# Performance work log

Measured on AMD Instinct MI355X. Metric: run time of the kernel, lower is better.

The kernel has to match this reference:

```python
import jax, jax.numpy as jnp
import numpy as np

N = 50000
E = 800000
NUM_GRAPHS = 128
X_IN, HID, EDGE_DIM = 64, 64, 16


def setup_inputs() -> dict:
    key = jax.random.key(0)
    ks = jax.random.split(key, 9)
    s = 0.05
    inp = {
        'x': jax.random.normal(ks[0], (N, X_IN), jnp.float32),
        'edge_index': jax.random.randint(ks[1], (2, E), 0, N, dtype=jnp.int32),
        'edge_attr': jax.random.normal(ks[2], (E, EDGE_DIM), jnp.float32),
        'batch': jnp.sort(jax.random.randint(ks[3], (N,), 0, NUM_GRAPHS, dtype=jnp.int32)),
        'w_fc1': jax.random.normal(ks[4], (EDGE_DIM, 1), jnp.float32) * s,
        'b_fc1': jnp.zeros((1,), jnp.float32),
    }
    dims = [(X_IN, HID), (HID, HID * 2), (HID * 2, HID)]
    for i, (din, dout) in enumerate(dims):
        k1, k2, k3 = jax.random.split(ks[5 + i], 3)
        inp[f'w1_{i}'] = jax.random.normal(k1, (din, dout), jnp.float32) * s
        inp[f'b1_{i}'] = jnp.zeros((dout,), jnp.float32)
        inp[f'w2_{i}'] = jax.random.normal(k2, (din, dout), jnp.float32) * s
        inp[f'w3_{i}'] = jax.random.normal(k3, (din, dout), jnp.float32) * s
        inp[f'b3_{i}'] = jnp.zeros((dout,), jnp.float32)
    return inp


def leconv(x, src, dst, ew, w1, b1, w2, w3, b3):
    # PyG LEConv: out_i = lin3(x_i) + sum_{j->i} e_ji * (lin1(x_j) - lin2(x_i))
    a = x @ w1 + b1          # lin1 (bias=True)   [N, out]
    b = x @ w2               # lin2 (bias=False)  [N, out]
    msg = ew[:, None] * (a[src] - b[dst])          # [E, out]
    agg = jax.ops.segment_sum(msg, dst, num_segments=N)
    return agg + x @ w3 + b3  # lin3 (bias=True)


def reference(x, edge_index, edge_attr, batch,
              w_fc1, b_fc1,
              w1_0, b1_0, w2_0, w3_0, b3_0,
              w1_1, b1_1, w2_1, w3_1, b3_1,
              w1_2, b1_2, w2_2, w3_2, b3_2):
    src, dst = edge_index[0], edge_index[1]
    ew = (edge_attr @ w_fc1 + b_fc1)[:, 0]         # fc1(edge_attr).squeeze(-1) -> [E]
    h = jax.nn.elu(leconv(x, src, dst, ew, w1_0, b1_0, w2_0, w3_0, b3_0))
    h = jax.nn.elu(leconv(h, src, dst, ew, w1_1, b1_1, w2_1, w3_1, b3_1))
    h = jax.nn.elu(leconv(h, src, dst, ew, w1_2, b1_2, w2_2, w3_2, b3_2))
    # global max pool over nodes of each graph -> [NUM_GRAPHS, HID]
    return jax.ops.segment_max(h, batch, num_segments=NUM_GRAPHS)
```

## Files before the change

### kernel.cpp

```cpp
#include <hip/hip_runtime.h>
#include <math.h>

#define N_NODES 50000
#define N_EDGES 800000
#define NUM_GRAPHS_ 128
#define SCAN_NB 98

typedef unsigned short u16;
typedef unsigned int u32;
typedef __attribute__((ext_vector_type(8))) short bf16x8;
typedef __attribute__((ext_vector_type(4))) float f32x4;

__device__ __forceinline__ float elu_f(float v) {
    return v > 0.f ? v : (__expf(v) - 1.f);
}
__device__ __forceinline__ u16 f2bf(float f) {
    u32 u = __float_as_uint(f);
    u += 0x7FFFu + ((u >> 16) & 1u);
    return (u16)(u >> 16);
}
__device__ __forceinline__ float bf2f(u16 h) {
    return __uint_as_float(((u32)h) << 16);
}
__device__ __forceinline__ void bfpair(u32 v, float& lo, float& hi) {
    lo = __uint_as_float(v << 16);
    hi = __uint_as_float(v & 0xFFFF0000u);
}
__device__ __forceinline__ u32 packbf(float lo, float hi) {
    return (u32)f2bf(lo) | ((u32)f2bf(hi) << 16);
}

__global__ void conv_x_kernel(const float* __restrict__ x, u16* __restrict__ xb) {
    int g = blockIdx.x * blockDim.x + threadIdx.x;
    float4 v = ((const float4*)x)[g];
    uint2 o;
    o.x = packbf(v.x, v.y);
    o.y = packbf(v.z, v.w);
    ((uint2*)xb)[g] = o;
}

__global__ void ew_deg_kernel(const float* __restrict__ edge_attr,
                              const float* __restrict__ w_fc1,
                              const float* __restrict__ b_fc1,
                              const int* __restrict__ edge_index,
                              float* __restrict__ ew,
                              int* __restrict__ deg) {
    int e = blockIdx.x * blockDim.x + threadIdx.x;
    if (e >= N_EDGES) return;
    const float4* ea = (const float4*)(edge_attr + (size_t)e * 16);
    const float4* wf = (const float4*)w_fc1;
    float acc = b_fc1[0];
#pragma unroll
    for (int i = 0; i < 4; i++) {
        float4 a = ea[i], w = wf[i];
        acc += a.x * w.x + a.y * w.y + a.z * w.z + a.w * w.w;
    }
    ew[e] = acc;
    atomicAdd(&deg[edge_index[N_EDGES + e]], 1);
}

__global__ void pack_w_kernel(const float* __restrict__ w3_0, const float* __restrict__ w1_0, const float* __restrict__ w2_0,
                              const float* __restrict__ w3_1, const float* __restrict__ w1_1, const float* __restrict__ w2_1,
                              const float* __restrict__ w3_2, const float* __restrict__ w1_2, const float* __restrict__ w2_2,
                              u16* __restrict__ bp0, u16* __restrict__ bp1, u16* __restrict__ bp2) {
    int t = blockIdx.x * blockDim.x + threadIdx.x;
    if (t >= 7680) return;
    int DIN, DOUT, lid;
    const float *w3, *w1, *w2;
    u16* bp;
    if (t < 1536)      { DIN = 64;  DOUT = 64;  lid = t;        w3 = w3_0; w1 = w1_0; w2 = w2_0; bp = bp0; }
    else if (t < 4608) { DIN = 64;  DOUT = 128; lid = t - 1536; w3 = w3_1; w1 = w1_1; w2 = w2_1; bp = bp1; }
    else               { DIN = 128; DOUT = 64;  lid = t - 4608; w3 = w3_2; w1 = w1_2; w2 = w2_2; bp = bp2; }
    const int NT = DOUT / 16;
    const int lane = lid & 63;
    const int fragid = lid >> 6;
    const int chunk = fragid / NT;
    const int ntile = fragid % NT;
    const int n = ntile * 16 + (lane & 15);
    const int kbase = chunk * 32 + (lane >> 4) * 8;
    u16 buf[8];
#pragma unroll
    for (int j = 0; j < 8; j++) {
        int k = kbase + j;
        int region = k / DIN;
        int kk = k - region * DIN;
        float v = (region == 0) ? w3[kk * DOUT + n]
                : (region == 1) ? w1[kk * DOUT + n]
                                : -w2[kk * DOUT + n];
        buf[j] = f2bf(v);
    }
    *(bf16x8*)(bp + ((size_t)lid << 3)) = *(bf16x8*)buf;
}

__global__ __launch_bounds__(256) void scan1_kernel(const int* __restrict__ deg,
                                                    int* __restrict__ rowptr,
                                                    int* __restrict__ blk_sums) {
    __shared__ int sh[256];
    const int t = threadIdx.x;
    const int base = blockIdx.x * 512;
    const int i0 = base + 2 * t, i1 = i0 + 1;
    const int d0 = (i0 < N_NODES) ? deg[i0] : 0;
    const int d1 = (i1 < N_NODES) ? deg[i1] : 0;
    const int pair = d0 + d1;
    int v = pair;
    sh[t] = v;
    __syncthreads();
#pragma unroll
    for (int off = 1; off < 256; off <<= 1) {
        int add = (t >= off) ? sh[t - off] : 0;
        __syncthreads();
        v += add;
        sh[t] = v;
        __syncthreads();
    }
    const int excl = v - pair;
    if (i0 < N_NODES) rowptr[i0] = excl;
    if (i1 < N_NODES) rowptr[i1] = excl + d0;
    if (t == 255) blk_sums[blockIdx.x] = v;
}

__global__ __launch_bounds__(128) void scan2_kernel(const int* __restrict__ blk_sums,
                                                    int* __restrict__ blk_offs,
                                                    int* __restrict__ rowptr) {
    __shared__ int sh[128];
    const int t = threadIdx.x;
    const int orig = (t < SCAN_NB) ? blk_sums[t] : 0;
    int v = orig;
    sh[t] = v;
    __syncthreads();
#pragma unroll
    for (int off = 1; off < 128; off <<= 1) {
        int add = (t >= off) ? sh[t - off] : 0;
        __syncthreads();
        v += add;
        sh[t] = v;
        __syncthreads();
    }
    if (t < SCAN_NB) blk_offs[t] = v - orig;
    if (t == 127) rowptr[N_NODES] = v;
}

__global__ void scan3_kernel(int* __restrict__ rowptr,
                             const int* __restrict__ blk_offs,
                             int* __restrict__ cursor) {
    int i = blockIdx.x * blockDim.x + threadIdx.x;
    if (i >= N_NODES) return;
    int r = rowptr[i] + blk_offs[i >> 9];
    rowptr[i] = r;
    cursor[i] = r;
}

__global__ void place_kernel(const int* __restrict__ edge_index,
                             const float* __restrict__ ew,
                             int* __restrict__ cursor,
                             int2* __restrict__ csr) {
    int e = blockIdx.x * blockDim.x + threadIdx.x;
    if (e >= N_EDGES) return;
    int dst = edge_index[N_EDGES + e];
    int pos = atomicAdd(&cursor[dst], 1);
    int2 ent;
    ent.x = edge_index[e];
    ent.y = __float_as_int(ew[e]);
    csr[pos] = ent;
}

template <int DIN, bool WRITE_C>
__global__ __launch_bounds__(256) void gather_kernel(
    const u16* __restrict__ xb, const int* __restrict__ rowptr,
    const int2* __restrict__ csr, u16* __restrict__ sb,
    u16* __restrict__ chb, float* __restrict__ c) {
    constexpr int CG = DIN / 4;
    constexpr int EG = 64 / CG;
    const int gid = blockIdx.x * 256 + threadIdx.x;
    const int node = gid >> 6;
    if (node >= N_NODES) return;
    const int lane = threadIdx.x & 63;
    const int cg = lane & (CG - 1);
    const int eg = lane / CG;
    const int beg = rowptr[node];
    const int end = rowptr[node + 1];
    const uint2* x2 = (const uint2*)xb;

    float a0 = 0.f, a1 = 0.f, a2 = 0.f, a3 = 0.f;
    float b0 = 0.f, b1 = 0.f, b2 = 0.f, b3 = 0.f;
    float wsum = 0.f;

    int p = beg + eg;
    for (; p + EG < end; p += 2 * EG) {
        int2 e0 = csr[p];
        int2 e1 = csr[p + EG];
        float w0 = __int_as_float(e0.y);
        float w1 = __int_as_float(e1.y);
        uint2 v0 = x2[(size_t)e0.x * CG + cg];
        uint2 v1 = x2[(size_t)e1.x * CG + cg];
        float f0, f1, f2, f3, g0, g1, g2, g3;
        bfpair(v0.x, f0, f1); bfpair(v0.y, f2, f3);
        bfpair(v1.x, g0, g1); bfpair(v1.y, g2, g3);
        a0 += w0 * f0; a1 += w0 * f1; a2 += w0 * f2; a3 += w0 * f3;
        b0 += w1 * g0; b1 += w1 * g1; b2 += w1 * g2; b3 += w1 * g3;
        wsum += w0 + w1;
    }
    if (p < end) {
        int2 e0 = csr[p];
        float w0 = __int_as_float(e0.y);
        uint2 v0 = x2[(size_t)e0.x * CG + cg];
        float f0, f1, f2, f3;
        bfpair(v0.x, f0, f1); bfpair(v0.y, f2, f3);
        a0 += w0 * f0; a1 += w0 * f1; a2 += w0 * f2; a3 += w0 * f3;
        wsum += w0;
    }
    a0 += b0; a1 += b1; a2 += b2; a3 += b3;

#pragma unroll
    for (int off = 32; off >= CG; off >>= 1) {
        a0 += __shfl_xor(a0, off);
        a1 += __shfl_xor(a1, off);
        a2 += __shfl_xor(a2, off);
        a3 += __shfl_xor(a3, off);
        wsum += __shfl_xor(wsum, off);
    }

    if (lane < CG) {
        uint2 so;
        so.x = packbf(a0, a1);
        so.y = packbf(a2, a3);
        ((uint2*)sb)[(size_t)node * CG + cg] = so;
        const float cn = WRITE_C ? wsum : c[node];
        uint2 hv = x2[(size_t)node * CG + cg];
        float h0, h1, h2, h3;
        bfpair(hv.x, h0, h1); bfpair(hv.y, h2, h3);
        uint2 co;
        co.x = packbf(cn * h0, cn * h1);
        co.y = packbf(cn * h2, cn * h3);
        ((uint2*)chb)[(size_t)node * CG + cg] = co;
    }
    if (WRITE_C && lane == 0) c[node] = wsum;
}

template <int DIN, int DOUT>
__global__ __launch_bounds__(256) void gemm_mfma(
    const u16* __restrict__ hb, const u16* __restrict__ sb,
    const u16* __restrict__ chb, const u16* __restrict__ Bp,
    const float* __restrict__ cvec, const float* __restrict__ bias1,
    const float* __restrict__ bias3, u16* __restrict__ outp) {
    constexpr int CH = DIN / 32;
    constexpr int CHUNKS = 3 * CH;
    constexpr int NT = DOUT / 16;
    const int tid = threadIdx.x;
    const int wv = tid >> 6;
    const int lane = tid & 63;
    const int l15 = lane & 15;
    const int q = lane >> 4;
    const int mhalf = wv & 1;
    const int nhalf = wv >> 1;
    const int row_base = blockIdx.x * 64 + mhalf * 32;
    const int nt0 = blockIdx.y * 4 + nhalf * 2;

    const int r0 = min(row_base + l15, N_NODES - 1);
    const int r1 = min(row_base + 16 + l15, N_NODES - 1);
    const int qo = q * 8;

    f32x4 acc00 = {0.f, 0.f, 0.f, 0.f};
    f32x4 acc01 = {0.f, 0.f, 0.f, 0.f};
    f32x4 acc10 = {0.f, 0.f, 0.f, 0.f};
    f32x4 acc11 = {0.f, 0.f, 0.f, 0.f};

#pragma unroll
    for (int chunk = 0; chunk < CHUNKS; chunk++) {
        const int region = chunk / CH;
        const int koff = (chunk - region * CH) * 32 + qo;
        const u16* A = (region == 0) ? hb : (region == 1) ? sb : chb;
        bf16x8 a0 = *(const bf16x8*)(A + (size_t)r0 * DIN + koff);
        bf16x8 a1 = *(const bf16x8*)(A + (size_t)r1 * DIN + koff);
        const u16* bp = Bp + (((size_t)(chunk * NT + nt0) * 64 + lane) << 3);
        bf16x8 bf0 = *(const bf16x8*)bp;
        bf16x8 bf1 = *(const bf16x8*)(bp + 64 * 8);
        acc00 = __builtin_amdgcn_mfma_f32_16x16x32_bf16(a0, bf0, acc00, 0, 0, 0);
        acc01 = __builtin_amdgcn_mfma_f32_16x16x32_bf16(a0, bf1, acc01, 0, 0, 0);
        acc10 = __builtin_amdgcn_mfma_f32_16x16x32_bf16(a1, bf0, acc10, 0, 0, 0);
        acc11 = __builtin_amdgcn_mfma_f32_16x16x32_bf16(a1, bf1, acc11, 0, 0, 0);
    }

#pragma unroll
    for (int ni = 0; ni < 2; ni++) {
        const int col = (nt0 + ni) * 16 + l15;
        const float B3 = bias3[col];
        const float B1 = bias1[col];
        const f32x4 am0 = ni ? acc01 : acc00;
        const f32x4 am1 = ni ? acc11 : acc10;
#pragma unroll
        for (int mi = 0; mi < 2; mi++) {
            const f32x4 av = mi ? am1 : am0;
#pragma unroll
            for (int reg = 0; reg < 4; reg++) {
                const int row = row_base + mi * 16 + q * 4 + reg;
                if (row < N_NODES) {
                    const float cv = cvec[row];
                    const float val = av[reg] + B3 + cv * B1;
                    outp[(size_t)row * DOUT + col] = f2bf(elu_f(val));
                }
            }
        }
    }
}

__global__ void pool_kernel(const u16* __restrict__ h,
                            const int* __restrict__ batch,
                            float* __restrict__ out) {
    const int g = blockIdx.x;
    const int tid = threadIdx.x;
    int lo = 0, hi = N_NODES;
    while (lo < hi) { int mid = (lo + hi) >> 1; if (batch[mid] < g) lo = mid + 1; else hi = mid; }
    const int beg = lo;
    lo = beg; hi = N_NODES;
    while (lo < hi) { int mid = (lo + hi) >> 1; if (batch[mid] < g + 1) lo = mid + 1; else hi = mid; }
    const int end = lo;

    __shared__ float red[256];
    const int col = tid & 63;
    const int rg = tid >> 6;
    float m = -3.0e38f;
    for (int r = beg + rg; r < end; r += 4) m = fmaxf(m, bf2f(h[(size_t)r * 64 + col]));
    red[tid] = m;
    __syncthreads();
    if (tid < 64) {
        m = fmaxf(fmaxf(red[tid], red[tid + 64]), fmaxf(red[tid + 128], red[tid + 192]));
        out[g * 64 + tid] = m;
    }
}

extern "C" void kernel_launch(void* const* d_in, const int* in_sizes, int n_in,
                              void* d_out, int out_size, void* d_ws, size_t ws_size,
                              hipStream_t stream) {
    const float* x = (const float*)d_in[0];
    const int* ei = (const int*)d_in[1];
    const float* ea = (const float*)d_in[2];
    const int* batch = (const int*)d_in[3];
    const float* wfc = (const float*)d_in[4];
    const float* bfc = (const float*)d_in[5];
    const float* w1_0 = (const float*)d_in[6];
    const float* b1_0 = (const float*)d_in[7];
    const float* w2_0 = (const float*)d_in[8];
    const float* w3_0 = (const float*)d_in[9];
    const float* b3_0 = (const float*)d_in[10];
    const float* w1_1 = (const float*)d_in[11];
    const float* b1_1 = (const float*)d_in[12];
    const float* w2_1 = (const float*)d_in[13];
    const float* w3_1 = (const float*)d_in[14];
    const float* b3_1 = (const float*)d_in[15];
    const float* w1_2 = (const float*)d_in[16];
    const float* b1_2 = (const float*)d_in[17];
    const float* w2_2 = (const float*)d_in[18];
    const float* w3_2 = (const float*)d_in[19];
    const float* b3_2 = (const float*)d_in[20];
    float* out = (float*)d_out;

    char* ws = (char*)d_ws;
    float* ew      = (float*)(ws);
    float* c       = (float*)(ws + 3200000);
    int*   deg     = (int*)  (ws + 3400000);
    int*   cursor  = (int*)  (ws + 3600000);
    int*   rowptr  = (int*)  (ws + 3800000);
    int2*  csr     = (int2*) (ws + 4000128);
    u16*   xb      = (u16*)  (ws + 10400128);
    u16*   sb      = (u16*)  (ws + 16800128);
    u16*   chb     = (u16*)  (ws + 29600128);
    u16*   h1      = (u16*)  (ws + 42400128);
    u16*   h2      = (u16*)  (ws + 48800128);
    u16*   h3      = (u16*)  (ws + 61600128);
    u16*   bp0     = (u16*)  (ws + 68000128);
    u16*   bp1     = (u16*)  (ws + 68024704);
    u16*   bp2     = (u16*)  (ws + 68073856);
    int* blk_sums  = (int*)  (ws + 68123008);
    int* blk_offs  = (int*)  (ws + 68123520);

    hipMemsetAsync(deg, 0, N_NODES * sizeof(int), stream);

    conv_x_kernel<<<3125, 256, 0, stream>>>(x, xb);
    ew_deg_kernel<<<(N_EDGES + 255) / 256, 256, 0, stream>>>(ea, wfc, bfc, ei, ew, deg);
    pack_w_kernel<<<30, 256, 0, stream>>>(w3_0, w1_0, w2_0, w3_1, w1_1, w2_1,
                                          w3_2, w1_2, w2_2, bp0, bp1, bp2);
    scan1_kernel<<<SCAN_NB, 256, 0, stream>>>(deg, rowptr, blk_sums);
    scan2_kernel<<<1, 128, 0, stream>>>(blk_sums, blk_offs, rowptr);
    scan3_kernel<<<(N_NODES + 255) / 256, 256, 0, stream>>>(rowptr, blk_offs, cursor);
    place_kernel<<<(N_EDGES + 255) / 256, 256, 0, stream>>>(ei, ew, cursor, csr);

    const int RB = (N_NODES + 63) / 64;
    const int GBLK = (N_NODES * 64 + 255) / 256;

    gather_kernel<64, true><<<GBLK, 256, 0, stream>>>(xb, rowptr, csr, sb, chb, c);
    gemm_mfma<64, 64><<<dim3(RB, 1), 256, 0, stream>>>(xb, sb, chb, bp0, c, b1_0, b3_0, h1);

    gather_kernel<64, false><<<GBLK, 256, 0, stream>>>(h1, rowptr, csr, sb, chb, c);
    gemm_mfma<64, 128><<<dim3(RB, 2), 256, 0, stream>>>(h1, sb, chb, bp1, c, b1_1, b3_1, h2);

    gather_kernel<128, false><<<GBLK, 256, 0, stream>>>(h2, rowptr, csr, sb, chb, c);
    gemm_mfma<128, 64><<<dim3(RB, 1), 256, 0, stream>>>(h2, sb, chb, bp2, c, b1_2, b3_2, h3);

    pool_kernel<<<NUM_GRAPHS_, 256, 0, stream>>>(h3, batch, out);
}
```

Measured before the change: 387.9 us.

## Partition CSR placement into destination-range passes with compact 16-bit dst array

The edge placement kernel now runs eight interleaved passes, each handling only edges whose destination falls in one node range. Each pass reads a 16-bit copy of the destination written by the edge-weight kernel. The aim is to confine the cursor atomics and CSR scatter writes to a smaller, cache-resident window and so improve locality. In exchange every edge's destination is read eight times and many more blocks are launched. The 16-bit copy is stored in the chb buffer before the first gather overwrites it, and it holds node IDs up to 49999, below 65536.

```diff
diff --git a/kernel.cpp b/kernel.cpp
--- a/kernel.cpp
+++ b/kernel.cpp
@@ -5,6 +5,8 @@
 #define N_EDGES 800000
 #define NUM_GRAPHS_ 128
 #define SCAN_NB 98
+#define NPASS 8
+#define NODES_PER_PASS 6250
 
 typedef unsigned short u16;
 typedef unsigned int u32;
@@ -44,6 +46,7 @@
                               const float* __restrict__ b_fc1,
                               const int* __restrict__ edge_index,
                               float* __restrict__ ew,
+                              u16* __restrict__ dst16,
                               int* __restrict__ deg) {
     int e = blockIdx.x * blockDim.x + threadIdx.x;
     if (e >= N_EDGES) return;
@@ -56,7 +59,165 @@
         acc += a.x * w.x + a.y * w.y + a.z * w.z + a.w * w.w;
     }
     ew[e] = acc;
-    atomicAdd(&deg[edge_index[N_EDGES + e]], 1);
+    int dst = edge_index[N_EDGES + e];
+    dst16[e] = (u16)dst;
+    atomicAdd(&deg[dst], 1);
+}
+
+__global__ __launch_bounds__(256) void scan1_kernel(const int* __restrict__ deg,
+                                                    int* __restrict__ rowptr,
+                                                    int* __restrict__ blk_sums) {
+    __shared__ int sh[256];
+    const int t = threadIdx.x;
+    const int base = blockIdx.x * 512;
+    const int i0 = base + 2 * t, i1 = i0 + 1;
+    const int d0 = (i0 < N_NODES) ? deg[i0] : 0;
+    const int d1 = (i1 < N_NODES) ? deg[i1] : 0;
+    const int pair = d0 + d1;
+    int v = pair;
+    sh[t] = v;
+    __syncthreads();
+#pragma unroll
+    for (int off = 1; off < 256; off <<= 1) {
+        int add = (t >= off) ? sh[t - off] : 0;
+        __syncthreads();
+        v += add;
+        sh[t] = v;
+        __syncthreads();
+    }
+    const int excl = v - pair;
+    if (i0 < N_NODES) rowptr[i0] = excl;
+    if (i1 < N_NODES) rowptr[i1] = excl + d0;
+    if (t == 255) blk_sums[blockIdx.x] = v;
+}
+
+__global__ __launch_bounds__(128) void scan2_kernel(const int* __restrict__ blk_sums,
+                                                    int* __restrict__ blk_offs,
+                                                    int* __restrict__ rowptr) {
+    __shared__ int sh[128];
+    const int t = threadIdx.x;
+    const int orig = (t < SCAN_NB) ? blk_sums[t] : 0;
+    int v = orig;
+    sh[t] = v;
+    __syncthreads();
+#pragma unroll
+    for (int off = 1; off < 128; off <<= 1) {
+        int add = (t >= off) ? sh[t - off] : 0;
+        __syncthreads();
+        v += add;
+        sh[t] = v;
+        __syncthreads();
+    }
+    if (t < SCAN_NB) blk_offs[t] = v - orig;
+    if (t == 127) rowptr[N_NODES] = v;
+}
+
+__global__ void scan3_kernel(int* __restrict__ rowptr,
+                             const int* __restrict__ blk_offs,
+                             int* __restrict__ cursor) {
+    int i = blockIdx.x * blockDim.x + threadIdx.x;
+    if (i >= N_NODES) return;
+    int r = rowptr[i] + blk_offs[i >> 9];
+    rowptr[i] = r;
+    cursor[i] = r;
+}
+
+__global__ __launch_bounds__(256) void place_kernel(const int* __restrict__ edge_index,
+                                                    const float* __restrict__ ew,
+                                                    const u16* __restrict__ dst16,
+                                                    int* __restrict__ cursor,
+                                                    int2* __restrict__ csr) {
+    const int pass = blockIdx.x & (NPASS - 1);
+    const int chunk = blockIdx.x >> 3;
+    const int lo = pass * NODES_PER_PASS;
+    const int hi = lo + NODES_PER_PASS;
+    const int base = chunk * 1024 + threadIdx.x;
+#pragma unroll
+    for (int u = 0; u < 4; u++) {
+        const int e = base + u * 256;
+        if (e >= N_EDGES) break;
+        const int d = (int)dst16[e];
+        if (d >= lo && d < hi) {
+            int pos = atomicAdd(&cursor[d], 1);
+            int2 ent;
+            ent.x = edge_index[e];
+            ent.y = __float_as_int(ew[e]);
+            csr[pos] = ent;
+        }
+    }
+}
+
+template <int DIN, bool WRITE_C>
+__global__ __launch_bounds__(256) void gather_kernel(
+    const u16* __restrict__ xb, const int* __restrict__ rowptr,
+    const int2* __restrict__ csr, u16* __restrict__ sb,
+    u16* __restrict__ chb, float* __restrict__ c) {
+    constexpr int CG = DIN / 4;
+    constexpr int EG = 64 / CG;
+    const int gid = blockIdx.x * 256 + threadIdx.x;
+    const int node = gid >> 6;
+    if (node >= N_NODES) return;
+    const int lane = threadIdx.x & 63;
+    const int cg = lane & (CG - 1);
+    const int eg = lane / CG;
+    const int beg = rowptr[node];
+    const int end = rowptr[node + 1];
+    const uint2* x2 = (const uint2*)xb;
+
+    float a0 = 0.f, a1 = 0.f, a2 = 0.f, a3 = 0.f;
+    float b0 = 0.f, b1 = 0.f, b2 = 0.f, b3 = 0.f;
+    float wsum = 0.f;
+
+    int p = beg + eg;
+    for (; p + EG < end; p += 2 * EG) {
+        int2 e0 = csr[p];
+        int2 e1 = csr[p + EG];
+        float w0 = __int_as_float(e0.y);
+        float w1 = __int_as_float(e1.y);
+        uint2 v0 = x2[(size_t)e0.x * CG + cg];
+        uint2 v1 = x2[(size_t)e1.x * CG + cg];
+        float f0, f1, f2, f3, g0, g1, g2, g3;
+        bfpair(v0.x, f0, f1); bfpair(v0.y, f2, f3);
+        bfpair(v1.x, g0, g1); bfpair(v1.y, g2, g3);
+        a0 += w0 * f0; a1 += w0 * f1; a2 += w0 * f2; a3 += w0 * f3;
+        b0 += w1 * g0; b1 += w1 * g1; b2 += w1 * g2; b3 += w1 * g3;
+        wsum += w0 + w1;
+    }
+    if (p < end) {
+        int2 e0 = csr[p];
+        float w0 = __int_as_float(e0.y);
+        uint2 v0 = x2[(size_t)e0.x * CG + cg];
+        float f0, f1, f2, f3;
+        bfpair(v0.x, f0, f1); bfpair(v0.y, f2, f3);
+        a0 += w0 * f0; a1 += w0 * f1; a2 += w0 * f2; a3 += w0 * f3;
+        wsum += w0;
+    }
+    a0 += b0; a1 += b1; a2 += b2; a3 += b3;
+
+#pragma unroll
+    for (int off = 32; off >= CG; off >>= 1) {
+        a0 += __shfl_xor(a0, off);
+        a1 += __shfl_xor(a1, off);
+        a2 += __shfl_xor(a2, off);
+        a3 += __shfl_xor(a3, off);
+        wsum += __shfl_xor(wsum, off);
+    }
+
+    if (lane < CG) {
+        uint2 so;
+        so.x = packbf(a0, a1);
+        so.y = packbf(a2, a3);
+        ((uint2*)sb)[(size_t)node * CG + cg] = so;
+        const float cn = WRITE_C ? wsum : c[node];
+        uint2 hv = x2[(size_t)node * CG + cg];
+        float h0, h1, h2, h3;
+        bfpair(hv.x, h0, h1); bfpair(hv.y, h2, h3);
+        uint2 co;
+        co.x = packbf(cn * h0, cn * h1);
+        co.y = packbf(cn * h2, cn * h3);
+        ((uint2*)chb)[(size_t)node * CG + cg] = co;
+    }
+    if (WRITE_C && lane == 0) c[node] = wsum;
 }
 
 __global__ void pack_w_kernel(const float* __restrict__ w3_0, const float* __restrict__ w1_0, const float* __restrict__ w2_0,
@@ -90,151 +251,6 @@
         buf[j] = f2bf(v);
     }
     *(bf16x8*)(bp + ((size_t)lid << 3)) = *(bf16x8*)buf;
-}
-
-__global__ __launch_bounds__(256) void scan1_kernel(const int* __restrict__ deg,
-                                                    int* __restrict__ rowptr,
-                                                    int* __restrict__ blk_sums) {
-    __shared__ int sh[256];
-    const int t = threadIdx.x;
-    const int base = blockIdx.x * 512;
-    const int i0 = base + 2 * t, i1 = i0 + 1;
-    const int d0 = (i0 < N_NODES) ? deg[i0] : 0;
-    const int d1 = (i1 < N_NODES) ? deg[i1] : 0;
-    const int pair = d0 + d1;
-    int v = pair;
-    sh[t] = v;
-    __syncthreads();
-#pragma unroll
-    for (int off = 1; off < 256; off <<= 1) {
-        int add = (t >= off) ? sh[t - off] : 0;
-        __syncthreads();
-        v += add;
-        sh[t] = v;
-        __syncthreads();
-    }
-    const int excl = v - pair;
-    if (i0 < N_NODES) rowptr[i0] = excl;
-    if (i1 < N_NODES) rowptr[i1] = excl + d0;
-    if (t == 255) blk_sums[blockIdx.x] = v;
-}
-
-__global__ __launch_bounds__(128) void scan2_kernel(const int* __restrict__ blk_sums,
-                                                    int* __restrict__ blk_offs,
-                                                    int* __restrict__ rowptr) {
-    __shared__ int sh[128];
-    const int t = threadIdx.x;
-    const int orig = (t < SCAN_NB) ? blk_sums[t] : 0;
-    int v = orig;
-    sh[t] = v;
-    __syncthreads();
-#pragma unroll
-    for (int off = 1; off < 128; off <<= 1) {
-        int add = (t >= off) ? sh[t - off] : 0;
-        __syncthreads();
-        v += add;
-        sh[t] = v;
-        __syncthreads();
-    }
-    if (t < SCAN_NB) blk_offs[t] = v - orig;
-    if (t == 127) rowptr[N_NODES] = v;
-}
-
-__global__ void scan3_kernel(int* __restrict__ rowptr,
-                             const int* __restrict__ blk_offs,
-                             int* __restrict__ cursor) {
-    int i = blockIdx.x * blockDim.x + threadIdx.x;
-    if (i >= N_NODES) return;
-    int r = rowptr[i] + blk_offs[i >> 9];
-    rowptr[i] = r;
-    cursor[i] = r;
-}
-
-__global__ void place_kernel(const int* __restrict__ edge_index,
-                             const float* __restrict__ ew,
-                             int* __restrict__ cursor,
-                             int2* __restrict__ csr) {
-    int e = blockIdx.x * blockDim.x + threadIdx.x;
-    if (e >= N_EDGES) return;
-    int dst = edge_index[N_EDGES + e];
-    int pos = atomicAdd(&cursor[dst], 1);
-    int2 ent;
-    ent.x = edge_index[e];
-    ent.y = __float_as_int(ew[e]);
-    csr[pos] = ent;
-}
-
-template <int DIN, bool WRITE_C>
-__global__ __launch_bounds__(256) void gather_kernel(
-    const u16* __restrict__ xb, const int* __restrict__ rowptr,
-    const int2* __restrict__ csr, u16* __restrict__ sb,
-    u16* __restrict__ chb, float* __restrict__ c) {
-    constexpr int CG = DIN / 4;
-    constexpr int EG = 64 / CG;
-    const int gid = blockIdx.x * 256 + threadIdx.x;
-    const int node = gid >> 6;
-    if (node >= N_NODES) return;
-    const int lane = threadIdx.x & 63;
-    const int cg = lane & (CG - 1);
-    const int eg = lane / CG;
-    const int beg = rowptr[node];
-    const int end = rowptr[node + 1];
-    const uint2* x2 = (const uint2*)xb;
-
-    float a0 = 0.f, a1 = 0.f, a2 = 0.f, a3 = 0.f;
-    float b0 = 0.f, b1 = 0.f, b2 = 0.f, b3 = 0.f;
-    float wsum = 0.f;
-
-    int p = beg + eg;
-    for (; p + EG < end; p += 2 * EG) {
-        int2 e0 = csr[p];
-        int2 e1 = csr[p + EG];
-        float w0 = __int_as_float(e0.y);
-        float w1 = __int_as_float(e1.y);
-        uint2 v0 = x2[(size_t)e0.x * CG + cg];
-        uint2 v1 = x2[(size_t)e1.x * CG + cg];
-        float f0, f1, f2, f3, g0, g1, g2, g3;
-        bfpair(v0.x, f0, f1); bfpair(v0.y, f2, f3);
-        bfpair(v1.x, g0, g1); bfpair(v1.y, g2, g3);
-        a0 += w0 * f0; a1 += w0 * f1; a2 += w0 * f2; a3 += w0 * f3;
-        b0 += w1 * g0; b1 += w1 * g1; b2 += w1 * g2; b3 += w1 * g3;
-        wsum += w0 + w1;
-    }
-    if (p < end) {
-        int2 e0 = csr[p];
-        float w0 = __int_as_float(e0.y);
-        uint2 v0 = x2[(size_t)e0.x * CG + cg];
-        float f0, f1, f2, f3;
-        bfpair(v0.x, f0, f1); bfpair(v0.y, f2, f3);
-        a0 += w0 * f0; a1 += w0 * f1; a2 += w0 * f2; a3 += w0 * f3;
-        wsum += w0;
-    }
-    a0 += b0; a1 += b1; a2 += b2; a3 += b3;
-
-#pragma unroll
-    for (int off = 32; off >= CG; off >>= 1) {
-        a0 += __shfl_xor(a0, off);
-        a1 += __shfl_xor(a1, off);
-        a2 += __shfl_xor(a2, off);
-        a3 += __shfl_xor(a3, off);
-        wsum += __shfl_xor(wsum, off);
-    }
-
-    if (lane < CG) {
-        uint2 so;
-        so.x = packbf(a0, a1);
-        so.y = packbf(a2, a3);
-        ((uint2*)sb)[(size_t)node * CG + cg] = so;
-        const float cn = WRITE_C ? wsum : c[node];
-        uint2 hv = x2[(size_t)node * CG + cg];
-        float h0, h1, h2, h3;
-        bfpair(hv.x, h0, h1); bfpair(hv.y, h2, h3);
-        uint2 co;
-        co.x = packbf(cn * h0, cn * h1);
-        co.y = packbf(cn * h2, cn * h3);
-        ((uint2*)chb)[(size_t)node * CG + cg] = co;
-    }
-    if (WRITE_C && lane == 0) c[node] = wsum;
 }
 
 template <int DIN, int DOUT>
@@ -373,17 +389,18 @@
     u16*   bp2     = (u16*)  (ws + 68073856);
     int* blk_sums  = (int*)  (ws + 68123008);
     int* blk_offs  = (int*)  (ws + 68123520);
+    u16* dst16 = chb;
 
     hipMemsetAsync(deg, 0, N_NODES * sizeof(int), stream);
 
     conv_x_kernel<<<3125, 256, 0, stream>>>(x, xb);
-    ew_deg_kernel<<<(N_EDGES + 255) / 256, 256, 0, stream>>>(ea, wfc, bfc, ei, ew, deg);
+    ew_deg_kernel<<<(N_EDGES + 255) / 256, 256, 0, stream>>>(ea, wfc, bfc, ei, ew, dst16, deg);
     pack_w_kernel<<<30, 256, 0, stream>>>(w3_0, w1_0, w2_0, w3_1, w1_1, w2_1,
                                           w3_2, w1_2, w2_2, bp0, bp1, bp2);
     scan1_kernel<<<SCAN_NB, 256, 0, stream>>>(deg, rowptr, blk_sums);
     scan2_kernel<<<1, 128, 0, stream>>>(blk_sums, blk_offs, rowptr);
     scan3_kernel<<<(N_NODES + 255) / 256, 256, 0, stream>>>(rowptr, blk_offs, cursor);
-    place_kernel<<<(N_EDGES + 255) / 256, 256, 0, stream>>>(ei, ew, cursor, csr);
+    place_kernel<<<782 * NPASS, 256, 0, stream>>>(ei, ew, dst16, cursor, csr);
 
     const int RB = (N_NODES + 63) / 64;
     const int GBLK = (N_NODES * 64 + 255) / 256;
```

New measurement: 383.4 us. About the same (-1.2%).
